# Optimization experiments

Measured on AMD Instinct MI355X. Metric: run time of the kernel, lower is better.

## Reference

```python
import jax, jax.numpy as jnp
import numpy as np

IOU_HI = 0.5
IOU_LO = 0.0
ROI_BS = 256
POS_RATIO = 0.25
BG = 20  # background class id; valid classes 0..BG-1
NUM_POS = int(ROI_BS * POS_RATIO)
DELTAS_SCALING = np.array([10.0, 10.0, 5.0, 5.0], dtype=np.float32)  # (x, y, w, h)


def _make_boxes(key, shape):
    ka, kb = jax.random.split(key)
    c = jax.random.uniform(ka, shape + (2,), minval=0.05, maxval=0.95)
    s = jax.random.uniform(kb, shape + (2,), minval=0.02, maxval=0.4)
    lo = jnp.clip(c - s / 2, 0.0, 1.0)
    hi = jnp.clip(c + s / 2, 0.0, 1.0)
    return jnp.concatenate([lo, hi], -1)  # (y1, x1, y2, x2), normalized


def setup_inputs() -> dict:
    key = jax.random.key(0)
    k1, k2, k3 = jax.random.split(key, 3)
    B, N, G = 32, 12000, 200
    rois = _make_boxes(k1, (B, N))
    gt_boxes = _make_boxes(k2, (B, G))
    # class == BG marks a padded / invalid GT box
    gt_class_ids = jax.random.randint(k3, (B, G), 0, BG + 1).astype(jnp.int32)
    return {"rois": rois, "gt_class_ids": gt_class_ids, "gt_boxes": gt_boxes}


def _iou(rois, gts):
    # rois [N,4], gts [G,4] in (y1,x1,y2,x2) -> [N,G]
    y1 = jnp.maximum(rois[:, None, 0], gts[None, :, 0])
    x1 = jnp.maximum(rois[:, None, 1], gts[None, :, 1])
    y2 = jnp.minimum(rois[:, None, 2], gts[None, :, 2])
    x2 = jnp.minimum(rois[:, None, 3], gts[None, :, 3])
    inter = jnp.clip(y2 - y1, 0.0) * jnp.clip(x2 - x1, 0.0)
    ar = (rois[:, 2] - rois[:, 0]) * (rois[:, 3] - rois[:, 1])
    ag = (gts[:, 2] - gts[:, 0]) * (gts[:, 3] - gts[:, 1])
    return inter / (ar[:, None] + ag[None, :] - inter + 1e-8)


def _encode(r, g):
    # (tx, ty, tw, th) * scaling, r/g: [K,4] in (y1,x1,y2,x2)
    eps = 1e-6
    rh = r[:, 2] - r[:, 0]; rw = r[:, 3] - r[:, 1]
    rcy = r[:, 0] + rh / 2; rcx = r[:, 1] + rw / 2
    gh = g[:, 2] - g[:, 0]; gw = g[:, 3] - g[:, 1]
    gcy = g[:, 0] + gh / 2; gcx = g[:, 1] + gw / 2
    tx = (gcx - rcx) / (rw + eps)
    ty = (gcy - rcy) / (rh + eps)
    tw = jnp.log(jnp.maximum(gw, eps) / (rw + eps))
    th = jnp.log(jnp.maximum(gh, eps) / (rh + eps))
    return jnp.stack([tx, ty, tw, th], -1) * jnp.asarray(DELTAS_SCALING)


def _per_image(rois, gt_cls, gt_boxes):
    iou = _iou(rois, gt_boxes)                       # [N,G]
    valid_gt = gt_cls < BG
    iou = jnp.where(valid_gt[None, :], iou, -1.0)
    max_iou = iou.max(1)                             # [N]
    best_gt = iou.argmax(1)                          # [N]
    pos = max_iou >= IOU_HI
    neg = (max_iou < IOU_HI) & (max_iou >= IOU_LO)

    # deterministic sampling: highest-IoU positives / negatives first
    pos_val, pos_idx = jax.lax.top_k(jnp.where(pos, max_iou, -1.0), NUM_POS)
    pos_ok = pos_val > 0.0
    neg_val, neg_idx = jax.lax.top_k(jnp.where(neg, max_iou + 2.0, -1.0), ROI_BS)
    neg_ok = neg_val > 0.0

    rP = jnp.arange(NUM_POS, dtype=jnp.float32)
    rN = jnp.arange(ROI_BS, dtype=jnp.float32)
    prio = jnp.concatenate([jnp.where(pos_ok, 1e9 - rP, -1e9 - rP),
                            jnp.where(neg_ok, 1e6 - rN, -1e6 - rN)])
    cand_idx = jnp.concatenate([pos_idx, neg_idx])
    cand_pos = jnp.concatenate([pos_ok, jnp.zeros(ROI_BS, bool)])
    _, sel = jax.lax.top_k(prio, ROI_BS)
    sel_roi = cand_idx[sel]                          # [ROI_BS]
    sel_is_pos = cand_pos[sel]                       # [ROI_BS]

    labels = jnp.where(sel_is_pos, gt_cls[best_gt[sel_roi]], BG)
    rois_sel = rois[sel_roi]                         # [ROI_BS,4]
    gts_sel = gt_boxes[best_gt[sel_roi]]             # [ROI_BS,4]
    t = _encode(rois_sel, gts_sel) * sel_is_pos[:, None].astype(rois.dtype)

    cls_onehot = jax.nn.one_hot(labels, BG + 1, dtype=rois.dtype)   # [ROI_BS,BG+1]
    onehot_fg = jax.nn.one_hot(labels, BG, dtype=rois.dtype)        # zero row for bg
    mask4 = jnp.repeat(onehot_fg, 4, axis=1)                        # [ROI_BS,4*BG]
    deltas_full = (onehot_fg[:, :, None] * t[:, None, :]).reshape(ROI_BS, 4 * BG)
    reg = jnp.concatenate([mask4, deltas_full], -1)                 # [ROI_BS,8*BG]
    return rois_sel, cls_onehot, reg


def reference(rois, gt_class_ids, gt_boxes):
    return jax.vmap(_per_image)(rois, gt_class_ids, gt_boxes)
```

## Files before the change

kernel.cpp:

```cpp
#include <hip/hip_runtime.h>
#include <stdint.h>

#pragma clang fp contract(off)

#define BATCH 32
#define NROI  12000
#define NGT   200
#define BGCLS 20
#define ROIBS 256
#define NPOS  64
#define NBIN  1024
#define CAP   2048
#define TSEL  1024
#define VPT2  12
#define HSH   16
#define HST   (NBIN + 2)
#define DELTA 1e-6f

__device__ __forceinline__ void roi_maxiou_all(const float4* cbox, const float* carea,
                                               int nv, float ry1, float rx1,
                                               float ry2, float rx2,
                                               float& best, int& bj) {
#pragma clang fp contract(off)
  float ar = (ry2 - ry1) * (rx2 - rx1);
  best = -1.0f; bj = 0;
#pragma unroll 4
  for (int j = 0; j < nv; ++j) {
    float4 q = cbox[j];
    float yy1 = fmaxf(ry1, q.x);
    float xx1 = fmaxf(rx1, q.y);
    float yy2 = fminf(ry2, q.z);
    float xx2 = fminf(rx2, q.w);
    float inter = fmaxf(yy2 - yy1, 0.0f) * fmaxf(xx2 - xx1, 0.0f);
    float den = ((ar + carea[j]) - inter) + 1e-8f;
    float iou = inter / den;
    if (iou > best) { best = iou; bj = j; }
  }
}

__device__ __forceinline__ float approx_max(const float4* cbox, const float* carea,
                                            int nv, float4 r) {
  float ar = (r.z - r.x) * (r.w - r.y);
  float va = -1.0f, vb = -1.0f;
#pragma unroll 4
  for (int j = 0; j < nv; ++j) {
    float4 q = cbox[j];
    float yy1 = fmaxf(r.x, q.x);
    float xx1 = fmaxf(r.y, q.y);
    float yy2 = fminf(r.z, q.z);
    float xx2 = fminf(r.w, q.w);
    float inter = fmaxf(yy2 - yy1, 0.0f) * fmaxf(xx2 - xx1, 0.0f);
    float den = ((ar + carea[j]) - inter) + 1e-8f;
    float a = inter * __builtin_amdgcn_rcpf(den);
    if (j & 1) vb = fmaxf(vb, a); else va = fmaxf(va, a);
  }
  return fmaxf(va, vb);
}

template <int NTHR>
__device__ __forceinline__ int stage_gt(float4* cbox, float* carea, int* ccls,
                                        int* snv, int* wtmp,
                                        const float* gtb, const int* gtc, int b) {
  const int tid = threadIdx.x;
  bool valid = false; float4 p = make_float4(0.f, 0.f, 0.f, 0.f); int cls = BGCLS;
  if (tid < NGT) {
    p = *(const float4*)(gtb + ((size_t)b * NGT + tid) * 4);
    cls = gtc[(size_t)b * NGT + tid];
    valid = (cls < BGCLS);
  }
  unsigned long long m = __ballot(valid);
  int w = tid >> 6;
  if ((tid & 63) == 0) wtmp[w] = __popcll(m);
  __syncthreads();
  if (tid == 0) {
    int s = 0;
    for (int i = 0; i < NTHR / 64; ++i) s += wtmp[i];
    *snv = s;
  }
  if (valid) {
    int off = 0;
    for (int i = 0; i < w; ++i) off += wtmp[i];
    int pos = off + __popcll(m & ((1ull << (tid & 63)) - 1ull));
    cbox[pos] = p;
    carea[pos] = (p.z - p.x) * (p.w - p.y);
    if (ccls) ccls[pos] = cls;
  }
  __syncthreads();
  return *snv;
}

__global__ __launch_bounds__(256) void k_ioumax(const float* __restrict__ rois,
                                                const int* __restrict__ gtc,
                                                const float* __restrict__ gtb,
                                                float* __restrict__ max_iou) {
  __shared__ float4 cbox[NGT];
  __shared__ float carea[NGT];
  __shared__ int snv, wtmp[4];
  const int b = blockIdx.y;
  const int nv = stage_gt<256>(cbox, carea, nullptr, &snv, wtmp, gtb, gtc, b);
  int n = blockIdx.x * 256 + threadIdx.x;
  if (n >= NROI) return;
  const float4 r = *(const float4*)(rois + ((size_t)b * NROI + n) * 4);
  max_iou[(size_t)b * NROI + n] = approx_max(cbox, carea, nv, r);
}

__global__ __launch_bounds__(TSEL) void k_selA(const float* __restrict__ rois,
                                               const int* __restrict__ gtc,
                                               const float* __restrict__ gtb,
                                               const float* __restrict__ mi,
                                               int* __restrict__ posCnt,
                                               int* __restrict__ posN,
                                               int* __restrict__ posBJ,
                                               int* __restrict__ negCnt,
                                               int* __restrict__ negN,
                                               int* __restrict__ negBJ) {
#pragma clang fp contract(off)
  __shared__ float4 cbox[NGT];
  __shared__ float carea[NGT];
  __shared__ int snv, wtmp[16];
  __shared__ int wtot[16], wnext[16];
  __shared__ int plist[CAP];
  __shared__ unsigned long long keyl[CAP];
  __shared__ int bjl[CAP];
  __shared__ int hs[HSH][HST];
  __shared__ int ss[NBIN];
  __shared__ int scnt, sX, sT, sOk;
  const int b = blockIdx.x >> 1;
  const bool isPos = (blockIdx.x & 1) == 0;
  const int tid = threadIdx.x;
  const int lane = tid & 63;
  const int nv = stage_gt<TSEL>(cbox, carea, nullptr, &snv, wtmp, gtb, gtc, b);

  float v[VPT2];
#pragma unroll
  for (int i = 0; i < VPT2; ++i) {
    int n = tid + (i << 10);
    v[i] = (n < NROI) ? mi[(size_t)b * NROI + n] : -3.0f;
  }

  auto mkbin = [](unsigned kh, unsigned base, int shift) -> int {
    int bin = ((int)(kh - base)) >> shift;
    return max(min(bin, NBIN - 1), 0);
  };
  const unsigned base = isPos ? 0x3F000000u : 0x40000000u;
  const int shift = isPos ? 13 : 11;

  for (int i = tid; i < HSH * HST; i += TSEL) ((int*)hs)[i] = 0;
  if (tid == 0) { scnt = 0; sX = 0; sOk = 0; }
  __syncthreads();
  const int sh = tid & (HSH - 1);
#pragma unroll
  for (int i = 0; i < VPT2; ++i) {
    int n = tid + (i << 10);
    float x = v[i];
    bool inb = isPos ? ((n < NROI) && (x >= 0.5f - DELTA))
                     : ((n < NROI) && (x < 0.5f + DELTA));
    if (inb) {
      unsigned kh = __float_as_uint(isPos ? x : (x + 2.0f));
      atomicAdd(&hs[sh][mkbin(kh, base, shift)], 1);
    }
    bool bnd = (n < NROI) && (x >= 0.5f - DELTA) && (x < 0.5f + DELTA);
    unsigned long long mx = __ballot(bnd);
    if (lane == 0 && mx) atomicAdd(&sX, __popcll(mx));
  }
  __syncthreads();
  const int limitWant = isPos ? NPOS : ROIBS;
  const int needv = limitWant + sX;

  {
    if (tid == 0) sT = 0;
    __syncthreads();
    int cnt_bin = 0;
#pragma unroll
    for (int i = 0; i < HSH; ++i) cnt_bin += hs[i][tid];
    const int w = tid >> 6;
    int sfx = cnt_bin;
#pragma unroll
    for (int off = 1; off < 64; off <<= 1) {
      int t = __shfl_down(sfx, off, 64);
      sfx += (lane + off < 64) ? t : 0;
    }
    if (lane == 0) wtot[w] = sfx;
    __syncthreads();
    if (tid < 16) {
      int s = 0;
      for (int i = tid + 1; i < 16; ++i) s += wtot[i];
      wnext[tid] = s;
    }
    __syncthreads();
    const int suffix = sfx + wnext[w];
    ss[tid] = suffix;
    __syncthreads();
    int nxt = (tid + 1 < NBIN) ? ss[tid + 1] : 0;
    if (suffix >= needv && nxt < needv) sT = tid;
    __syncthreads();
  }
  const int Tc = max(sT - 2, 0);

#pragma unroll
  for (int i = 0; i < VPT2; ++i) {
    int n = tid + (i << 10);
    float x = v[i];
    bool inb = isPos ? ((n < NROI) && (x >= 0.5f - DELTA))
                     : ((n < NROI) && (x < 0.5f + DELTA));
    bool pred = inb &&
        (mkbin(__float_as_uint(isPos ? x : (x + 2.0f)), base, shift) >= Tc);
    unsigned long long mk = __ballot(pred);
    int c = __popcll(mk);
    int bs = 0;
    if (lane == 0 && c) bs = atomicAdd(&scnt, c);
    bs = __shfl(bs, 0, 64);
    if (pred) {
      int idx = bs + __popcll(mk & ((1ull << lane) - 1ull));
      if (idx < CAP) plist[idx] = n;
    }
  }
  __syncthreads();
  const int cnt = min(scnt, CAP);

  for (int i = tid; i < cnt; i += TSEL) {
    int n = plist[i];
    const float4 r = *(const float4*)(rois + ((size_t)b * NROI + n) * 4);
    float best; int bj;
    roi_maxiou_all(cbox, carea, nv, r.x, r.y, r.z, r.w, best, bj);
    bool ok = isPos ? (best >= 0.5f) : (best < 0.5f);
    unsigned kh = __float_as_uint(isPos ? best : (best + 2.0f));
    keyl[i] = ok ? (((unsigned long long)kh << 32) | (unsigned)(0x7fffffff - n))
                 : 0ull;
    bjl[i] = bj;
    if (ok) atomicAdd(&sOk, 1);
  }
  __syncthreads();
  const int limit = min(sOk, limitWant);
  if (tid == 0) { if (isPos) posCnt[b] = limit; else negCnt[b] = limit; }

  int* dstN = isPos ? (posN + (size_t)b * NPOS) : (negN + (size_t)b * ROIBS);
  int* dstB = isPos ? (posBJ + (size_t)b * NPOS) : (negBJ + (size_t)b * ROIBS);
  for (int i = tid; i < cnt; i += TSEL) {
    unsigned long long ki = keyl[i];
    if (ki) {
      int r0 = 0, r1 = 0, r2 = 0, r3 = 0;
      int j = 0;
      for (; j + 4 <= cnt; j += 4) {
        r0 += (keyl[j + 0] > ki);
        r1 += (keyl[j + 1] > ki);
        r2 += (keyl[j + 2] > ki);
        r3 += (keyl[j + 3] > ki);
      }
      for (; j < cnt; ++j) r0 += (keyl[j] > ki);
      int rank = r0 + r1 + r2 + r3;
      if (rank < limit) {
        dstN[rank] = 0x7fffffff - (int)(ki & 0xffffffffu);
        dstB[rank] = bjl[i];
      }
    }
  }
}

__global__ __launch_bounds__(TSEL) void k_emit(const float* __restrict__ rois,
                                               const int* __restrict__ gtc,
                                               const float* __restrict__ gtb,
                                               const int* __restrict__ posCnt,
                                               const int* __restrict__ posN,
                                               const int* __restrict__ posBJ,
                                               const int* __restrict__ negCnt,
                                               const int* __restrict__ negN,
                                               const int* __restrict__ negBJ,
                                               float* __restrict__ out) {
#pragma clang fp contract(off)
  __shared__ float4 cbox[NGT];
  __shared__ float carea[NGT];
  __shared__ int ccls[NGT];
  __shared__ int snv, wtmp[16];
  const int b = blockIdx.x;
  const int tid = threadIdx.x;
  stage_gt<TSEL>(cbox, carea, ccls, &snv, wtmp, gtb, gtc, b);

  const int P = min(posCnt[b], NPOS);
  const int NC = negCnt[b];
  const int slot = tid >> 2, q = tid & 3;
  int r = 0, bj = 0, isp = 0;
  if (slot < P) {
    r = posN[(size_t)b * NPOS + slot];
    bj = posBJ[(size_t)b * NPOS + slot];
    isp = 1;
  } else {
    int j = slot - P;
    if (j < NC) {
      r = negN[(size_t)b * ROIBS + j];
      bj = negBJ[(size_t)b * ROIBS + j];
    }
  }
  const float4 rv = *(const float4*)(rois + ((size_t)b * NROI + r) * 4);
  float ry1 = rv.x, rx1 = rv.y, ry2 = rv.z, rx2 = rv.w;
  int label = isp ? ccls[bj] : BGCLS;

  float* out1 = out;
  float* out2 = out + (size_t)BATCH * ROIBS * 4;
  float* out3 = out + (size_t)BATCH * ROIBS * 25;
  size_t row = (size_t)b * ROIBS + slot;

  if (q == 0) {
    *(float4*)(out1 + row * 4) = rv;
    float* o2 = out2 + row * 21;
    for (int c = 0; c <= BGCLS; ++c) o2[c] = (c == label) ? 1.0f : 0.0f;
  }

  float t0 = 0.f, t1 = 0.f, t2 = 0.f, t3 = 0.f;
  if (isp) {
    const float eps = 1e-6f;
    float4 g = cbox[bj];
    float rh = ry2 - ry1, rw = rx2 - rx1;
    float rcy = ry1 + rh * 0.5f, rcx = rx1 + rw * 0.5f;
    float gh = g.z - g.x, gw = g.w - g.y;
    float gcy = g.x + gh * 0.5f, gcx = g.y + gw * 0.5f;
    t0 = ((gcx - rcx) / (rw + eps)) * 10.0f;
    t1 = ((gcy - rcy) / (rh + eps)) * 10.0f;
    t2 = logf(fmaxf(gw, eps) / (rw + eps)) * 5.0f;
    t3 = logf(fmaxf(gh, eps) / (rh + eps)) * 5.0f;
  }
  int m0 = label * 4;
  float* o3 = out3 + row * 160;
  for (int c = q * 10; c < q * 10 + 10; ++c) {
    float4 wv = make_float4(0.f, 0.f, 0.f, 0.f);
    if (isp) {
      float* wp = &wv.x;
#pragma unroll
      for (int jj = 0; jj < 4; ++jj) {
        int e = c * 4 + jj;
        float x = 0.f;
        if (e >= m0 && e < m0 + 4) x = 1.0f;
        int d = e - 80 - m0;
        if (d == 0) x = t0; else if (d == 1) x = t1;
        else if (d == 2) x = t2; else if (d == 3) x = t3;
        wp[jj] = x;
      }
    }
    *(float4*)(o3 + c * 4) = wv;
  }
}

__global__ __launch_bounds__(TSEL) void k_sel_mono(const float* __restrict__ rois,
                                                   const int* __restrict__ gtc,
                                                   const float* __restrict__ gtb,
                                                   float* __restrict__ out) {
#pragma clang fp contract(off)
  __shared__ float4 cbox[NGT];
  __shared__ float carea[NGT];
  __shared__ int ccls[NGT];
  __shared__ int snv, wtmp[16];
  __shared__ int wtot[16], wnext[16];
  __shared__ int plist[CAP];
  __shared__ unsigned long long keyl[CAP];
  __shared__ int bjl[CAP];
  __shared__ int hs[HSH][HST];
  __shared__ int ss[NBIN];
  __shared__ int sel_r[ROIBS];
  __shared__ int sel_b[ROIBS];
  __shared__ int scnt, sX, sT, sPos;
  const int b = blockIdx.x;
  const int tid = threadIdx.x;
  const int lane = tid & 63;
  if (tid < ROIBS) { sel_r[tid] = 0; sel_b[tid] = 0; }
  const int nv = stage_gt<TSEL>(cbox, carea, ccls, &snv, wtmp, gtb, gtc, b);

  float v[VPT2];
#pragma unroll
  for (int i = 0; i < VPT2; ++i) {
    int n = tid + (i << 10);
    if (n < NROI) {
      const float4 r = *(const float4*)(rois + ((size_t)b * NROI + n) * 4);
      v[i] = approx_max(cbox, carea, nv, r);
    } else v[i] = -3.0f;
  }

  auto mkbin = [](unsigned kh, unsigned base, int shift) -> int {
    int bin = ((int)(kh - base)) >> shift;
    return max(min(bin, NBIN - 1), 0);
  };
  auto find_T = [&](int needv) -> int {
    if (tid == 0) sT = 0;
    __syncthreads();
    int cnt_bin = 0;
#pragma unroll
    for (int i = 0; i < HSH; ++i) cnt_bin += hs[i][tid];
    const int w = tid >> 6;
    int sfx = cnt_bin;
#pragma unroll
    for (int off = 1; off < 64; off <<= 1) {
      int t = __shfl_down(sfx, off, 64);
      sfx += (lane + off < 64) ? t : 0;
    }
    if (lane == 0) wtot[w] = sfx;
    __syncthreads();
    if (tid < 16) {
      int s = 0;
      for (int i = tid + 1; i < 16; ++i) s += wtot[i];
      wnext[tid] = s;
    }
    __syncthreads();
    const int suffix = sfx + wnext[w];
    ss[tid] = suffix;
    __syncthreads();
    int nxt = (tid + 1 < NBIN) ? ss[tid + 1] : 0;
    if (suffix >= needv && nxt < needv) sT = tid;
    __syncthreads();
    return sT;
  };
  auto rank_of = [&](unsigned long long ki, int cnt) -> int {
    int r0 = 0, r1 = 0, r2 = 0, r3 = 0;
    int j = 0;
    for (; j + 4 <= cnt; j += 4) {
      r0 += (keyl[j + 0] > ki);
      r1 += (keyl[j + 1] > ki);
      r2 += (keyl[j + 2] > ki);
      r3 += (keyl[j + 3] > ki);
    }
    for (; j < cnt; ++j) r0 += (keyl[j] > ki);
    return r0 + r1 + r2 + r3;
  };
  const int sh = tid & (HSH - 1);

  for (int i = tid; i < HSH * HST; i += TSEL) ((int*)hs)[i] = 0;
  if (tid == 0) { scnt = 0; sX = 0; sPos = 0; }
  __syncthreads();
#pragma unroll
  for (int i = 0; i < VPT2; ++i) {
    int n = tid + (i << 10);
    float x = v[i];
    bool inb = (n < NROI) && (x >= 0.5f - DELTA);
    if (inb) atomicAdd(&hs[sh][mkbin(__float_as_uint(x), 0x3F000000u, 13)], 1);
    bool bnd = inb && (x < 0.5f + DELTA);
    unsigned long long mx = __ballot(bnd);
    if (lane == 0 && mx) atomicAdd(&sX, __popcll(mx));
  }
  __syncthreads();
  const int XB = sX;
  const int Tp = max(find_T(NPOS + XB) - 2, 0);
#pragma unroll
  for (int i = 0; i < VPT2; ++i) {
    int n = tid + (i << 10);
    float x = v[i];
    bool pred = (n < NROI) && (x >= 0.5f - DELTA) &&
                (mkbin(__float_as_uint(x), 0x3F000000u, 13) >= Tp);
    unsigned long long mk = __ballot(pred);
    int c = __popcll(mk);
    int bs = 0;
    if (lane == 0 && c) bs = atomicAdd(&scnt, c);
    bs = __shfl(bs, 0, 64);
    if (pred) {
      int idx = bs + __popcll(mk & ((1ull << lane) - 1ull));
      if (idx < CAP) plist[idx] = n;
    }
  }
  __syncthreads();
  const int cntp = min(scnt, CAP);
  for (int i = tid; i < cntp; i += TSEL) {
    int n = plist[i];
    const float4 r = *(const float4*)(rois + ((size_t)b * NROI + n) * 4);
    float best; int bj;
    roi_maxiou_all(cbox, carea, nv, r.x, r.y, r.z, r.w, best, bj);
    bool ok = (best >= 0.5f);
    keyl[i] = ok ? (((unsigned long long)__float_as_uint(best) << 32)
                   | (unsigned)(0x7fffffff - n)) : 0ull;
    bjl[i] = bj;
    if (ok) atomicAdd(&sPos, 1);
  }
  __syncthreads();
  const int P = min(sPos, NPOS);
  for (int i = tid; i < cntp; i += TSEL) {
    unsigned long long ki = keyl[i];
    if (ki) {
      int rank = rank_of(ki, cntp);
      if (rank < P) {
        sel_r[rank] = 0x7fffffff - (int)(ki & 0xffffffffu);
        sel_b[rank] = bjl[i];
      }
    }
  }
  __syncthreads();

  const int need = ROIBS - P;
  for (int i = tid; i < HSH * HST; i += TSEL) ((int*)hs)[i] = 0;
  if (tid == 0) scnt = 0;
  __syncthreads();
#pragma unroll
  for (int i = 0; i < VPT2; ++i) {
    int n = tid + (i << 10);
    float x = v[i];
    if (n < NROI && x < 0.5f + DELTA)
      atomicAdd(&hs[sh][mkbin(__float_as_uint(x + 2.0f), 0x40000000u, 11)], 1);
  }
  __syncthreads();
  const int Tn = max(find_T(need + XB) - 2, 0);
#pragma unroll
  for (int i = 0; i < VPT2; ++i) {
    int n = tid + (i << 10);
    float x = v[i];
    bool pred = (n < NROI) && (x < 0.5f + DELTA) &&
                (mkbin(__float_as_uint(x + 2.0f), 0x40000000u, 11) >= Tn);
    unsigned long long mk = __ballot(pred);
    int c = __popcll(mk);
    int bs = 0;
    if (lane == 0 && c) bs = atomicAdd(&scnt, c);
    bs = __shfl(bs, 0, 64);
    if (pred) {
      int idx = bs + __popcll(mk & ((1ull << lane) - 1ull));
      if (idx < CAP) plist[idx] = n;
    }
  }
  __syncthreads();
  const int cntn = min(scnt, CAP);
  for (int i = tid; i < cntn; i += TSEL) {
    int n = plist[i];
    const float4 r = *(const float4*)(rois + ((size_t)b * NROI + n) * 4);
    float best; int bj;
    roi_maxiou_all(cbox, carea, nv, r.x, r.y, r.z, r.w, best, bj);
    bool ok = (best < 0.5f);
    keyl[i] = ok ? (((unsigned long long)__float_as_uint(best + 2.0f) << 32)
                   | (unsigned)(0x7fffffff - n)) : 0ull;
    bjl[i] = bj;
  }
  __syncthreads();
  for (int i = tid; i < cntn; i += TSEL) {
    unsigned long long ki = keyl[i];
    if (ki) {
      int rank = rank_of(ki, cntn);
      if (rank < need) {
        sel_r[P + rank] = 0x7fffffff - (int)(ki & 0xffffffffu);
        sel_b[P + rank] = bjl[i];
      }
    }
  }
  __syncthreads();

  {
    const int slot = tid >> 2, q = tid & 3;
    const int r = sel_r[slot];
    const int bj = sel_b[slot];
    const int isp = (slot < P) ? 1 : 0;
    const float4 rv = *(const float4*)(rois + ((size_t)b * NROI + r) * 4);
    float ry1 = rv.x, rx1 = rv.y, ry2 = rv.z, rx2 = rv.w;
    int label = isp ? ccls[bj] : BGCLS;
    float* out1 = out;
    float* out2 = out + (size_t)BATCH * ROIBS * 4;
    float* out3 = out + (size_t)BATCH * ROIBS * 25;
    size_t row = (size_t)b * ROIBS + slot;
    if (q == 0) {
      *(float4*)(out1 + row * 4) = rv;
      float* o2 = out2 + row * 21;
      for (int c = 0; c <= BGCLS; ++c) o2[c] = (c == label) ? 1.0f : 0.0f;
    }
    float t0 = 0.f, t1 = 0.f, t2 = 0.f, t3 = 0.f;
    if (isp) {
      const float eps = 1e-6f;
      float4 g = cbox[bj];
      float rh = ry2 - ry1, rw = rx2 - rx1;
      float rcy = ry1 + rh * 0.5f, rcx = rx1 + rw * 0.5f;
      float gh = g.z - g.x, gw = g.w - g.y;
      float gcy = g.x + gh * 0.5f, gcx = g.y + gw * 0.5f;
      t0 = ((gcx - rcx) / (rw + eps)) * 10.0f;
      t1 = ((gcy - rcy) / (rh + eps)) * 10.0f;
      t2 = logf(fmaxf(gw, eps) / (rw + eps)) * 5.0f;
      t3 = logf(fmaxf(gh, eps) / (rh + eps)) * 5.0f;
    }
    int m0 = label * 4;
    float* o3 = out3 + row * 160;
    for (int c = q * 10; c < q * 10 + 10; ++c) {
      float4 wv = make_float4(0.f, 0.f, 0.f, 0.f);
      if (isp) {
        float* wp = &wv.x;
#pragma unroll
        for (int jj = 0; jj < 4; ++jj) {
          int e = c * 4 + jj;
          float x = 0.f;
          if (e >= m0 && e < m0 + 4) x = 1.0f;
          int d = e - 80 - m0;
          if (d == 0) x = t0; else if (d == 1) x = t1;
          else if (d == 2) x = t2; else if (d == 3) x = t3;
          wp[jj] = x;
        }
      }
      *(float4*)(o3 + c * 4) = wv;
    }
  }
}

extern "C" void kernel_launch(void* const* d_in, const int* in_sizes, int n_in,
                              void* d_out, int out_size, void* d_ws, size_t ws_size,
                              hipStream_t stream) {
  const float* rois = (const float*)d_in[0];
  const int*   gtc  = (const int*)d_in[1];
  const float* gtb  = (const float*)d_in[2];
  float*       out  = (float*)d_out;

  const size_t A = (size_t)BATCH * NROI;
  const size_t nint = 32 + (size_t)BATCH * NPOS * 2 + 32 + (size_t)BATCH * ROIBS * 2;
  const size_t need = (A + nint) * 4;
  if (d_ws && ws_size >= need) {
    float* mi = (float*)d_ws;
    int* p = (int*)((float*)d_ws + A);
    int* posCnt = p;             p += 32;
    int* posN   = p;             p += BATCH * NPOS;
    int* posBJ  = p;             p += BATCH * NPOS;
    int* negCnt = p;             p += 32;
    int* negN   = p;             p += BATCH * ROIBS;
    int* negBJ  = p;
    k_ioumax<<<dim3((NROI + 255) / 256, BATCH), 256, 0, stream>>>(rois, gtc, gtb, mi);
    k_selA<<<BATCH * 2, TSEL, 0, stream>>>(rois, gtc, gtb, mi,
                                           posCnt, posN, posBJ,
                                           negCnt, negN, negBJ);
    k_emit<<<BATCH, TSEL, 0, stream>>>(rois, gtc, gtb, posCnt, posN, posBJ,
                                       negCnt, negN, negBJ, out);
  } else {
    k_sel_mono<<<BATCH, TSEL, 0, stream>>>(rois, gtc, gtb, out);
  }
}
```

Measured before the change: 86.34 us.

## Precompact valid GT boxes in a separate kernel and read them from global memory in IoU-max

Adds a small kernel that compacts the valid GT boxes and their areas per image into workspace once. The IoU-max kernel then reads these uniform values straight from global or scalar memory, with no per-block LDS staging and no barrier. It also inlines the IoU loop using a hardware reciprocal and two alternating max accumulators. The cost is one extra kernel launch, and the approximate reciprocal may change which max IoU values fall on either side of the thresholds.

```diff
diff --git a/kernel.cpp b/kernel.cpp
--- a/kernel.cpp
+++ b/kernel.cpp
@@ -89,19 +89,62 @@
   return *snv;
 }
 
+__global__ __launch_bounds__(256) void k_gtstage(const int* __restrict__ gtc,
+                                                 const float* __restrict__ gtb,
+                                                 float4* __restrict__ gbox,
+                                                 float* __restrict__ garea,
+                                                 int* __restrict__ gnv) {
+#pragma clang fp contract(off)
+  __shared__ int wtmp[4];
+  const int b = blockIdx.x;
+  const int tid = threadIdx.x;
+  bool valid = false; float4 p = make_float4(0.f, 0.f, 0.f, 0.f);
+  if (tid < NGT) {
+    p = *(const float4*)(gtb + ((size_t)b * NGT + tid) * 4);
+    valid = gtc[(size_t)b * NGT + tid] < BGCLS;
+  }
+  unsigned long long m = __ballot(valid);
+  int w = tid >> 6;
+  if ((tid & 63) == 0) wtmp[w] = __popcll(m);
+  __syncthreads();
+  if (tid == 0) gnv[b] = wtmp[0] + wtmp[1] + wtmp[2] + wtmp[3];
+  if (valid) {
+    int off = 0;
+    for (int i = 0; i < w; ++i) off += wtmp[i];
+    int pos = off + __popcll(m & ((1ull << (tid & 63)) - 1ull));
+    gbox[(size_t)b * NGT + pos] = p;
+    garea[(size_t)b * NGT + pos] = (p.z - p.x) * (p.w - p.y);
+  }
+}
+
 __global__ __launch_bounds__(256) void k_ioumax(const float* __restrict__ rois,
-                                                const int* __restrict__ gtc,
-                                                const float* __restrict__ gtb,
+                                                const float4* __restrict__ gbox,
+                                                const float* __restrict__ garea,
+                                                const int* __restrict__ gnv,
                                                 float* __restrict__ max_iou) {
-  __shared__ float4 cbox[NGT];
-  __shared__ float carea[NGT];
-  __shared__ int snv, wtmp[4];
   const int b = blockIdx.y;
-  const int nv = stage_gt<256>(cbox, carea, nullptr, &snv, wtmp, gtb, gtc, b);
+  const int nv = gnv[b];
+  const float4* __restrict__ gb = gbox + (size_t)b * NGT;
+  const float*  __restrict__ ga = garea + (size_t)b * NGT;
   int n = blockIdx.x * 256 + threadIdx.x;
   if (n >= NROI) return;
   const float4 r = *(const float4*)(rois + ((size_t)b * NROI + n) * 4);
-  max_iou[(size_t)b * NROI + n] = approx_max(cbox, carea, nv, r);
+  const float ar = (r.z - r.x) * (r.w - r.y);
+  float va = -1.0f, vb = -1.0f;
+#pragma unroll 4
+  for (int j = 0; j < nv; ++j) {
+    float4 q = gb[j];
+    float ag = ga[j];
+    float yy1 = fmaxf(r.x, q.x);
+    float xx1 = fmaxf(r.y, q.y);
+    float yy2 = fminf(r.z, q.z);
+    float xx2 = fminf(r.w, q.w);
+    float inter = fmaxf(yy2 - yy1, 0.0f) * fmaxf(xx2 - xx1, 0.0f);
+    float den = ((ar + ag) - inter) + 1e-8f;
+    float a = inter * __builtin_amdgcn_rcpf(den);
+    if (j & 1) vb = fmaxf(vb, a); else va = fmaxf(va, a);
+  }
+  max_iou[(size_t)b * NROI + n] = fmaxf(va, vb);
 }
 
 __global__ __launch_bounds__(TSEL) void k_selA(const float* __restrict__ rois,
@@ -595,18 +638,23 @@
   float*       out  = (float*)d_out;
 
   const size_t A = (size_t)BATCH * NROI;
-  const size_t nint = 32 + (size_t)BATCH * NPOS * 2 + 32 + (size_t)BATCH * ROIBS * 2;
-  const size_t need = (A + nint) * 4;
+  const size_t GB4 = (size_t)BATCH * NGT;
+  const size_t nint = 32 + (size_t)BATCH * NPOS * 2 + 32 + (size_t)BATCH * ROIBS * 2 + 32;
+  const size_t need = A * 4 + GB4 * 16 + GB4 * 4 + nint * 4;
   if (d_ws && ws_size >= need) {
     float* mi = (float*)d_ws;
-    int* p = (int*)((float*)d_ws + A);
+    float4* gbox = (float4*)(mi + A);
+    float* garea = (float*)(gbox + GB4);
+    int* p = (int*)(garea + GB4);
+    int* gnv    = p;             p += 32;
     int* posCnt = p;             p += 32;
     int* posN   = p;             p += BATCH * NPOS;
     int* posBJ  = p;             p += BATCH * NPOS;
     int* negCnt = p;             p += 32;
     int* negN   = p;             p += BATCH * ROIBS;
     int* negBJ  = p;
-    k_ioumax<<<dim3((NROI + 255) / 256, BATCH), 256, 0, stream>>>(rois, gtc, gtb, mi);
+    k_gtstage<<<BATCH, 256, 0, stream>>>(gtc, gtb, gbox, garea, gnv);
+    k_ioumax<<<dim3((NROI + 255) / 256, BATCH), 256, 0, stream>>>(rois, gbox, garea, gnv, mi);
     k_selA<<<BATCH * 2, TSEL, 0, stream>>>(rois, gtc, gtb, mi,
                                            posCnt, posN, posBJ,
                                            negCnt, negN, negBJ);
```

Measured after the change: 95.78 us. 1.11x slower.
